# Kernel tuning notes

Hardware: AMD Instinct MI355X
Metric: run time of the kernel (lower is better)

## Reference

```python
import jax, jax.numpy as jnp
import numpy as np
from jax import lax

B, C, H, W = 32, 684, 16, 64
HID, A, CK, K = 256, 512, 512, 11


def setup_inputs() -> dict:
    key = jax.random.key(0)
    ks = jax.random.split(key, 12)
    s = 0.02
    return {
        "cnn_features": jax.random.normal(ks[0], (B, C, H, W), jnp.float32),
        "hidden": jax.random.normal(ks[1], (B, HID), jnp.float32),
        "alpha_sum": jax.random.uniform(ks[2], (B, 1, H, W), jnp.float32),
        "image_mask": jnp.ones((B, 1, H, W), jnp.float32),
        # hidden_weight: Linear(HID -> A)
        "Wh": jax.random.normal(ks[3], (A, HID), jnp.float32) * s,
        "bh": jnp.zeros((A,), jnp.float32),
        # encoder_feature_conv: Conv2d(C -> A, 1x1) == pointwise linear
        "Wec": jax.random.normal(ks[4], (A, C), jnp.float32) * s,
        "bec": jnp.zeros((A,), jnp.float32),
        # attention_conv: Conv2d(1 -> CK, 11x11, pad 5, no bias)
        "Wac": jax.random.normal(ks[5], (CK, 1, K, K), jnp.float32) * s,
        # attention_weight: Linear(CK -> A, no bias)
        "Waw": jax.random.normal(ks[6], (A, CK), jnp.float32) * s,
        # alpha_convert: Linear(A -> 1)
        "Wv": jax.random.normal(ks[7], (1, A), jnp.float32) * s,
        "bv": jnp.zeros((1,), jnp.float32),
    }


def reference(cnn_features, hidden, alpha_sum, image_mask,
              Wh, bh, Wec, bec, Wac, Waw, Wv, bv):
    # query = hidden_weight(hidden): [B, A]
    query = hidden @ Wh.T + bh
    # attention_conv(alpha_sum): [B, CK, H, W]
    ast = lax.conv_general_dilated(
        alpha_sum, Wac, window_strides=(1, 1),
        padding=[(K // 2, K // 2), (K // 2, K // 2)],
        dimension_numbers=("NCHW", "OIHW", "NCHW"))
    # attention_weight on permuted conv output: [B, H, W, A]
    coverage_alpha = jnp.einsum("bkhw,ak->bhwa", ast, Waw)
    # encoder_feature_conv (1x1 conv == pointwise linear): [B, H, W, A]
    cnn_trans = jnp.einsum("bchw,ac->bhwa", cnn_features, Wec) + bec
    # additive attention score
    alpha_score = jnp.tanh(query[:, None, None, :] + coverage_alpha + cnn_trans)
    # alpha_convert -> scalar energy per position: [B, H, W]
    energy = jnp.einsum("bhwa,a->bhw", alpha_score, Wv[0]) + bv[0]
    energy = energy - energy.max()  # global max-subtract as in original
    energy_exp = jnp.exp(energy) * image_mask[:, 0]
    denom = energy_exp.sum(axis=(-1, -2))[:, None, None] + 1e-10
    alpha = energy_exp / denom  # [B, H, W]
    alpha_sum_new = alpha[:, None, :, :] + alpha_sum  # [B, 1, H, W]
    # context: weighted spatial sum over features -> [B, C]
    context_vector = jnp.einsum("bhw,bchw->bc", alpha, cnn_features)
    return (context_vector, alpha, alpha_sum_new)
```

## Files before the change

### kernel.cpp

```cpp
#include <hip/hip_runtime.h>
#include <math.h>

#define Bn   32
#define Cn   684
#define Hn   16
#define Wn   64
#define HWn  1024
#define HIDn 256
#define An   512
#define KKn  121
#define CREAL 805
#define CPAD 832
#define NSTEP 26
#define NBLK 256

#define OUT_ALPHA 21888
#define OUT_ASUM  (21888 + 32768)

typedef short short8 __attribute__((ext_vector_type(8)));
typedef float floatx4 __attribute__((ext_vector_type(4)));

__device__ __forceinline__ unsigned short f2bf(float f) {
    union { float f; unsigned int i; } v; v.f = f;
    unsigned int i = v.i;
    return (unsigned short)((i + 0x7fffu + ((i >> 16) & 1u)) >> 16);
}
__device__ __forceinline__ unsigned int pack2bf(float v0, float v1) {
    unsigned int u0 = __float_as_uint(v0), u1 = __float_as_uint(v1);
    u0 = (u0 + 0x7fffu + ((u0 >> 16) & 1u)) >> 16;
    u1 = (u1 + 0x7fffu + ((u1 >> 16) & 1u)) & 0xffff0000u;
    return u0 | u1;
}
__device__ __forceinline__ void async_lds16(void* lds, const void* g) {
    __builtin_amdgcn_global_load_lds(
        (const __attribute__((address_space(1))) unsigned int*)g,
        (__attribute__((address_space(3))) unsigned int*)lds, 16, 0, 0);
}

__global__ __launch_bounds__(256) void k_prep(
    const float* __restrict__ hidden,
    const float* __restrict__ Wh,
    const float* __restrict__ bh,
    const float* __restrict__ bec,
    const float* __restrict__ Wec,
    const float* __restrict__ Wac,
    const float* __restrict__ Waw,
    float* __restrict__ query,
    unsigned short* __restrict__ VTbf)
{
    __shared__ float sbuf[512];
    const int blk = blockIdx.x, t = threadIdx.x;
    if (blk < 512) {
        const int a = blk;
        sbuf[t]       = Waw[(size_t)a * 512 + t];
        sbuf[t + 256] = Waw[(size_t)a * 512 + t + 256];
        __syncthreads();
        for (int cp = t; cp < Cn; cp += 256)
            VTbf[(size_t)a * CPAD + cp] = f2bf(Wec[(size_t)a * Cn + cp]);
        if (t < KKn) {
            float s = 0.f;
            #pragma unroll 8
            for (int k = 0; k < 512; ++k)
                s = fmaf(sbuf[k], Wac[k * KKn + t], s);
            VTbf[(size_t)a * CPAD + Cn + t] = f2bf(s);
        }
        for (int cp = CREAL + t; cp < CPAD; cp += 256)
            VTbf[(size_t)a * CPAD + cp] = 0;
    } else {
        const int b = blk - 512;
        sbuf[t] = (t < HIDn) ? hidden[b * HIDn + t] : 0.f;
        __syncthreads();
        for (int a = t; a < An; a += 256) {
            const float4* wp = (const float4*)(Wh + (size_t)a * HIDn);
            float s = bh[a] + bec[a];
            #pragma unroll 8
            for (int i = 0; i < HIDn / 4; ++i) {
                float4 w = wp[i];
                s = fmaf(sbuf[4 * i],     w.x, s);
                s = fmaf(sbuf[4 * i + 1], w.y, s);
                s = fmaf(sbuf[4 * i + 2], w.z, s);
                s = fmaf(sbuf[4 * i + 3], w.w, s);
            }
            query[b * An + a] = s;
        }
    }
}

__device__ __forceinline__ float fetchU(const float* __restrict__ X,
                                        const float* plane,
                                        int m, int row) {
    if (row < Cn)   return X[(size_t)row * HWn + m];
    if (row < CREAL) {
        int ij = row - Cn; int di = ij / 11, dj = ij - di * 11;
        return plane[di * 74 + m + dj];
    }
    return 0.f;
}

__global__ __launch_bounds__(256, 3) void k_energy(
    const float* __restrict__ X,
    const float* __restrict__ asum,
    const float* __restrict__ Wv,
    const float* __restrict__ query,
    const unsigned short* __restrict__ VTbf,
    float* __restrict__ energy)
{
    __shared__ __align__(16) unsigned short As[2 * 64 * 40];
    __shared__ __align__(16) unsigned short Bs[2 * 256 * 32];
    __shared__ float plane[11 * 74 + 2];
    __shared__ float qs[NBLK];
    __shared__ float wvs[NBLK];

    const int t = threadIdx.x;
    const int nh = blockIdx.x, hh = blockIdx.y, b = blockIdx.z;
    const int w = t >> 6, lane = t & 63;
    const int q = lane >> 4, r = lane & 15;
    const int nbase = nh * NBLK;
    const int mA = t & 63;
    const int koA = t >> 6;

    const float* Xb = X + (size_t)b * Cn * HWn + hh * Wn;

    const int gcw = (lane & 3) ^ ((lane >> 2) & 3) ^ ((lane >> 4) & 3);

    for (int i = t; i < 11 * 74; i += 256) {
        int di = i / 74, cc = i - di * 74;
        int h2 = hh + di - 5, w2 = cc - 5;
        float v = 0.f;
        if (h2 >= 0 && h2 < Hn && w2 >= 0 && w2 < Wn)
            v = asum[b * HWn + h2 * Wn + w2];
        plane[i] = v;
    }
    qs[t]  = query[b * An + nbase + t];
    wvs[t] = Wv[nbase + t];
    {
        const float* xp = Xb + (size_t)(koA * 8) * HWn + mA;
        unsigned int pk[4];
        #pragma unroll
        for (int jj = 0; jj < 4; ++jj)
            pk[jj] = pack2bf(xp[(size_t)(2 * jj) * HWn], xp[(size_t)(2 * jj + 1) * HWn]);
        *(uint4*)&As[mA * 40 + koA * 8] = make_uint4(pk[0], pk[1], pk[2], pk[3]);
    }
    #pragma unroll
    for (int ii = 0; ii < 4; ++ii) {
        int n0 = w * 64 + ii * 16;
        int row = nbase + n0 + (lane >> 2);
        async_lds16(&Bs[n0 * 32], VTbf + (size_t)row * CPAD + gcw * 8);
    }
    __syncthreads();

    floatx4 acc[4][4];
    #pragma unroll
    for (int mf = 0; mf < 4; ++mf)
        #pragma unroll
        for (int nf = 0; nf < 4; ++nf)
            acc[mf][nf] = (floatx4){0.f, 0.f, 0.f, 0.f};

    for (int ch = 0; ch < NSTEP; ++ch) {
        const int cur = ch & 1;
        const unsigned short* Ab = As + cur * (64 * 40);
        const unsigned short* Bb = Bs + cur * (256 * 32);

        short8 af[4], bfr[4];
        #pragma unroll
        for (int mf = 0; mf < 4; ++mf)
            af[mf] = *(const short8*)&Ab[(mf * 16 + r) * 40 + q * 8];
        #pragma unroll
        for (int nf = 0; nf < 4; ++nf)
            bfr[nf] = *(const short8*)&Bb[(w * 64 + nf * 16 + r) * 32 +
                                          ((q ^ (r & 3) ^ ((r >> 2) & 3)) * 8)];

        const bool stage = (ch < NSTEP - 1);
        float av[8];
        if (stage) {
            const int c1 = (ch + 1) * 32;
            if (c1 + 31 < Cn) {
                const float* xp = Xb + (size_t)(c1 + koA * 8) * HWn + mA;
                #pragma unroll
                for (int jj = 0; jj < 8; ++jj)
                    av[jj] = xp[(size_t)jj * HWn];
            } else {
                #pragma unroll
                for (int jj = 0; jj < 8; ++jj)
                    av[jj] = fetchU(Xb, plane, mA, c1 + koA * 8 + jj);
            }
            unsigned short* Bn_ = Bs + (cur ^ 1) * (256 * 32);
            #pragma unroll
            for (int ii = 0; ii < 4; ++ii) {
                int n0 = w * 64 + ii * 16;
                int row = nbase + n0 + (lane >> 2);
                async_lds16(&Bn_[n0 * 32], VTbf + (size_t)row * CPAD + c1 + gcw * 8);
            }
        }

        #pragma unroll
        for (int mf = 0; mf < 4; ++mf)
            #pragma unroll
            for (int nf = 0; nf < 4; ++nf)
                acc[mf][nf] = __builtin_amdgcn_mfma_f32_16x16x32_bf16(
                    af[mf], bfr[nf], acc[mf][nf], 0, 0, 0);

        if (stage) {
            unsigned int pk[4];
            #pragma unroll
            for (int jj = 0; jj < 4; ++jj)
                pk[jj] = pack2bf(av[2 * jj], av[2 * jj + 1]);
            *(uint4*)&As[(cur ^ 1) * (64 * 40) + mA * 40 + koA * 8] =
                make_uint4(pk[0], pk[1], pk[2], pk[3]);
        }

        __syncthreads();
    }

    float ep[16];
    #pragma unroll
    for (int i = 0; i < 16; ++i) ep[i] = 0.f;
    #pragma unroll
    for (int nf = 0; nf < 4; ++nf) {
        int nl = w * 64 + nf * 16 + r;
        float qv = qs[nl], wv = wvs[nl];
        #pragma unroll
        for (int mf = 0; mf < 4; ++mf)
            #pragma unroll
            for (int rg = 0; rg < 4; ++rg) {
                float x = acc[mf][nf][rg] + qv;
                float e2 = __expf(2.f * x);
                float th = 1.f - 2.f * __builtin_amdgcn_rcpf(e2 + 1.f);
                ep[mf * 4 + rg] += wv * th;
            }
    }
    float* red = (float*)Bs;
    #pragma unroll
    for (int mf = 0; mf < 4; ++mf)
        #pragma unroll
        for (int rg = 0; rg < 4; ++rg)
            red[(mf * 16 + q * 4 + rg) * 65 + w * 16 + r] = ep[mf * 4 + rg];
    __syncthreads();
    if (t < 64) {
        float s = 0.f;
        #pragma unroll 16
        for (int i = 0; i < 64; ++i) s += red[t * 65 + i];
        atomicAdd(&energy[b * HWn + hh * Wn + t], s);
    }
}

__global__ __launch_bounds__(256) void k_softmax(
    const float* __restrict__ mask,
    const float* __restrict__ asum,
    float* __restrict__ energy,
    float* __restrict__ out)
{
    __shared__ float rsm[8];
    const int b = blockIdx.x;
    const int t = threadIdx.x, lane = t & 63, wid = t >> 6;

    float e[4], ex[4];
    #pragma unroll
    for (int i = 0; i < 4; ++i) e[i] = energy[b * HWn + i * 256 + t];
    float m = fmaxf(fmaxf(e[0], e[1]), fmaxf(e[2], e[3]));
    for (int off = 32; off >= 1; off >>= 1) m = fmaxf(m, __shfl_down(m, off, 64));
    if (lane == 0) rsm[wid] = m;
    __syncthreads();
    if (t == 0)
        rsm[4] = fmaxf(fmaxf(rsm[0], rsm[1]), fmaxf(rsm[2], rsm[3]));
    __syncthreads();
    const float M = rsm[4];
    float s = 0.f;
    #pragma unroll
    for (int i = 0; i < 4; ++i) {
        ex[i] = expf(e[i] - M) * mask[b * HWn + i * 256 + t];
        s += ex[i];
    }
    for (int off = 32; off >= 1; off >>= 1) s += __shfl_down(s, off, 64);
    __syncthreads();
    if (lane == 0) rsm[wid] = s;
    __syncthreads();
    if (t == 0) rsm[5] = rsm[0] + rsm[1] + rsm[2] + rsm[3] + 1e-10f;
    __syncthreads();
    const float denom = rsm[5];
    #pragma unroll
    for (int i = 0; i < 4; ++i) {
        int p = i * 256 + t;
        float a = ex[i] / denom;
        energy[b * HWn + p] = a;
        out[OUT_ALPHA + b * HWn + p] = a;
        out[OUT_ASUM  + b * HWn + p] = a + asum[b * HWn + p];
    }
}

__global__ __launch_bounds__(256) void k_ctx(
    const float* __restrict__ X,
    const float* __restrict__ alpha,
    float* __restrict__ out)
{
    __shared__ float al[1024];
    const int bx = blockIdx.x, b = blockIdx.y;
    const int t = threadIdx.x, lane = t & 63, wid = t >> 6;

    #pragma unroll
    for (int i = 0; i < 4; ++i) al[i * 256 + t] = alpha[b * HWn + i * 256 + t];
    __syncthreads();

    const int c = bx * 4 + wid;
    const float* xp = X + ((size_t)(b * Cn + c)) * HWn;
    float s2 = 0.f;
    #pragma unroll
    for (int i = 0; i < 4; ++i) {
        int off = i * 256 + lane * 4;
        float4 x = *(const float4*)(xp + off);
        float4 a = *(const float4*)(al + off);
        s2 = fmaf(a.x, x.x, s2);
        s2 = fmaf(a.y, x.y, s2);
        s2 = fmaf(a.z, x.z, s2);
        s2 = fmaf(a.w, x.w, s2);
    }
    for (int off = 32; off >= 1; off >>= 1) s2 += __shfl_down(s2, off, 64);
    if (lane == 0) out[b * Cn + c] = s2;
}

extern "C" void kernel_launch(void* const* d_in, const int* in_sizes, int n_in,
                              void* d_out, int out_size, void* d_ws, size_t ws_size,
                              hipStream_t stream)
{
    const float* X      = (const float*)d_in[0];
    const float* hidden = (const float*)d_in[1];
    const float* asum   = (const float*)d_in[2];
    const float* mask   = (const float*)d_in[3];
    const float* Wh     = (const float*)d_in[4];
    const float* bh     = (const float*)d_in[5];
    const float* Wec    = (const float*)d_in[6];
    const float* bec    = (const float*)d_in[7];
    const float* Wac    = (const float*)d_in[8];
    const float* Waw    = (const float*)d_in[9];
    const float* Wv     = (const float*)d_in[10];
    (void)in_sizes; (void)n_in; (void)out_size; (void)ws_size;

    float* out = (float*)d_out;
    float* ws = (float*)d_ws;
    float* query  = ws;
    float* energy = ws + 16384;
    unsigned short* VTbf = (unsigned short*)(ws + 16384 + 32768);

    hipMemsetAsync(energy, 0, HWn * Bn * sizeof(float), stream);
    k_prep    <<<dim3(544),       dim3(256), 0, stream>>>(hidden, Wh, bh, bec,
                                                          Wec, Wac, Waw, query, VTbf);
    k_energy  <<<dim3(2, 16, 32), dim3(256), 0, stream>>>(X, asum, Wv, query, VTbf, energy);
    k_softmax <<<dim3(32),        dim3(256), 0, stream>>>(mask, asum, energy, out);
    k_ctx     <<<dim3(171, 32),   dim3(256), 0, stream>>>(X, energy, out);
}
```

Measured before the change: 272.6 us.

## Load B fragments directly from pre-swizzled global layout and remove block barriers

The prep kernel now writes the bf16 weight matrix in an MFMA fragment-ordered layout, so the energy kernel loads B fragments straight from global memory into registers instead of staging them through LDS. Each wave now stages its own copy of the A tile (all 64 positions by 32 channels) in a private LDS region, using float4 loads, which removes the per-step block-wide __syncthreads. The main loop is manually double-buffered in registers and LDS. The grid is flattened so the two N-halves of the same (b,h) tile run on adjacent blocks, sharing X reads through L2. The trade-off is four times the X loads and conversions per block, and more register pressure.

```diff
diff --git a/kernel.cpp b/kernel.cpp
--- a/kernel.cpp
+++ b/kernel.cpp
@@ -1,4 +1,5 @@
 #include <hip/hip_runtime.h>
+#include <hip/hip_bf16.h>
 #include <math.h>
 
 #define Bn   32
@@ -25,16 +26,15 @@
     unsigned int i = v.i;
     return (unsigned short)((i + 0x7fffu + ((i >> 16) & 1u)) >> 16);
 }
-__device__ __forceinline__ unsigned int pack2bf(float v0, float v1) {
-    unsigned int u0 = __float_as_uint(v0), u1 = __float_as_uint(v1);
-    u0 = (u0 + 0x7fffu + ((u0 >> 16) & 1u)) >> 16;
-    u1 = (u1 + 0x7fffu + ((u1 >> 16) & 1u)) & 0xffff0000u;
-    return u0 | u1;
-}
-__device__ __forceinline__ void async_lds16(void* lds, const void* g) {
-    __builtin_amdgcn_global_load_lds(
-        (const __attribute__((address_space(1))) unsigned int*)g,
-        (__attribute__((address_space(3))) unsigned int*)lds, 16, 0, 0);
+__device__ __forceinline__ unsigned int cvt2(float lo, float hi) {
+    __hip_bfloat162 h = __float22bfloat162_rn(float2{lo, hi});
+    union { __hip_bfloat162 h; unsigned int u; } cv; cv.h = h;
+    return cv.u;
+}
+
+__device__ __forceinline__ size_t bfr_idx(int n, int k) {
+    return ((((size_t)(n >> 4) * 26 + (k >> 5)) * 64
+             + ((k >> 3) & 3) * 16 + (n & 15)) * 8) + (k & 7);
 }
 
 __global__ __launch_bounds__(256) void k_prep(
@@ -46,7 +46,7 @@
     const float* __restrict__ Wac,
     const float* __restrict__ Waw,
     float* __restrict__ query,
-    unsigned short* __restrict__ VTbf)
+    unsigned short* __restrict__ Bfr)
 {
     __shared__ float sbuf[512];
     const int blk = blockIdx.x, t = threadIdx.x;
@@ -56,16 +56,16 @@
         sbuf[t + 256] = Waw[(size_t)a * 512 + t + 256];
         __syncthreads();
         for (int cp = t; cp < Cn; cp += 256)
-            VTbf[(size_t)a * CPAD + cp] = f2bf(Wec[(size_t)a * Cn + cp]);
+            Bfr[bfr_idx(a, cp)] = f2bf(Wec[(size_t)a * Cn + cp]);
         if (t < KKn) {
             float s = 0.f;
             #pragma unroll 8
             for (int k = 0; k < 512; ++k)
                 s = fmaf(sbuf[k], Wac[k * KKn + t], s);
-            VTbf[(size_t)a * CPAD + Cn + t] = f2bf(s);
+            Bfr[bfr_idx(a, Cn + t)] = f2bf(s);
         }
         for (int cp = CREAL + t; cp < CPAD; cp += 256)
-            VTbf[(size_t)a * CPAD + cp] = 0;
+            Bfr[bfr_idx(a, cp)] = 0;
     } else {
         const int b = blk - 512;
         sbuf[t] = (t < HIDn) ? hidden[b * HIDn + t] : 0.f;
@@ -86,42 +86,31 @@
     }
 }
 
-__device__ __forceinline__ float fetchU(const float* __restrict__ X,
-                                        const float* plane,
-                                        int m, int row) {
-    if (row < Cn)   return X[(size_t)row * HWn + m];
-    if (row < CREAL) {
-        int ij = row - Cn; int di = ij / 11, dj = ij - di * 11;
-        return plane[di * 74 + m + dj];
-    }
-    return 0.f;
-}
-
 __global__ __launch_bounds__(256, 3) void k_energy(
     const float* __restrict__ X,
     const float* __restrict__ asum,
     const float* __restrict__ Wv,
     const float* __restrict__ query,
-    const unsigned short* __restrict__ VTbf,
+    const unsigned short* __restrict__ Bfr,
     float* __restrict__ energy)
 {
-    __shared__ __align__(16) unsigned short As[2 * 64 * 40];
-    __shared__ __align__(16) unsigned short Bs[2 * 256 * 32];
+    __shared__ __align__(16) unsigned int As[4][2][64 * 20];
     __shared__ float plane[11 * 74 + 2];
     __shared__ float qs[NBLK];
     __shared__ float wvs[NBLK];
 
     const int t = threadIdx.x;
-    const int nh = blockIdx.x, hh = blockIdx.y, b = blockIdx.z;
+    const int d = blockIdx.x;
+    const int nh  = (d >> 3) & 1;
+    const int pid = (d >> 4) * 8 + (d & 7);
+    const int hh = pid & 15, b = pid >> 4;
     const int w = t >> 6, lane = t & 63;
     const int q = lane >> 4, r = lane & 15;
     const int nbase = nh * NBLK;
-    const int mA = t & 63;
-    const int koA = t >> 6;
+    const int mg = lane & 15, kg = lane >> 4;
 
     const float* Xb = X + (size_t)b * Cn * HWn + hh * Wn;
-
-    const int gcw = (lane & 3) ^ ((lane >> 2) & 3) ^ ((lane >> 4) & 3);
+    const unsigned short* Bp = Bfr + (size_t)(nh * 16 + w * 4) * 26 * 512;
 
     for (int i = t; i < 11 * 74; i += 256) {
         int di = i / 74, cc = i - di * 74;
@@ -133,21 +122,70 @@
     }
     qs[t]  = query[b * An + nbase + t];
     wvs[t] = Wv[nbase + t];
-    {
-        const float* xp = Xb + (size_t)(koA * 8) * HWn + mA;
-        unsigned int pk[4];
-        #pragma unroll
-        for (int jj = 0; jj < 4; ++jj)
-            pk[jj] = pack2bf(xp[(size_t)(2 * jj) * HWn], xp[(size_t)(2 * jj + 1) * HWn]);
-        *(uint4*)&As[mA * 40 + koA * 8] = make_uint4(pk[0], pk[1], pk[2], pk[3]);
-    }
-    #pragma unroll
-    for (int ii = 0; ii < 4; ++ii) {
-        int n0 = w * 64 + ii * 16;
-        int row = nbase + n0 + (lane >> 2);
-        async_lds16(&Bs[n0 * 32], VTbf + (size_t)row * CPAD + gcw * 8);
-    }
-    __syncthreads();
+    __syncthreads();
+
+    unsigned int* A0 = &As[w][0][0];
+    unsigned int* A1 = &As[w][1][0];
+
+    __align__(16) float va[32];
+    short8 b0[4], b1[4], af[4];
+
+#define LOADX(CH) {                                                           \
+    const int c0 = (CH) * 32 + kg * 8;                                        \
+    if (c0 + 7 < Cn) {                                                        \
+        const float* xp = Xb + (size_t)c0 * HWn + mg * 4;                     \
+        _Pragma("unroll")                                                     \
+        for (int j = 0; j < 8; ++j)                                           \
+            *(float4*)&va[j * 4] = *(const float4*)(xp + (size_t)j * HWn);    \
+    } else {                                                                  \
+        _Pragma("unroll")                                                     \
+        for (int j = 0; j < 8; ++j) {                                         \
+            const int row = c0 + j;                                           \
+            _Pragma("unroll")                                                 \
+            for (int mm = 0; mm < 4; ++mm) {                                  \
+                float vv = 0.f;                                               \
+                if (row < Cn) vv = Xb[(size_t)row * HWn + mg * 4 + mm];       \
+                else if (row < CREAL) {                                       \
+                    int ij = row - Cn; int di = ij / 11, dj = ij - di * 11;   \
+                    vv = plane[di * 74 + mg * 4 + mm + dj];                   \
+                }                                                             \
+                va[j * 4 + mm] = vv;                                          \
+            }                                                                 \
+        }                                                                     \
+    } }
+
+#define CVTWR(DST) {                                                          \
+    _Pragma("unroll")                                                         \
+    for (int mi = 0; mi < 4; ++mi) {                                          \
+        uint4 u;                                                              \
+        u.x = cvt2(va[0 * 4 + mi], va[1 * 4 + mi]);                           \
+        u.y = cvt2(va[2 * 4 + mi], va[3 * 4 + mi]);                           \
+        u.z = cvt2(va[4 * 4 + mi], va[5 * 4 + mi]);                           \
+        u.w = cvt2(va[6 * 4 + mi], va[7 * 4 + mi]);                           \
+        *(uint4*)&(DST)[(mg * 4 + mi) * 20 + kg * 4] = u;                     \
+    } }
+
+#define LOADB(DSTB, CH) {                                                     \
+    _Pragma("unroll")                                                         \
+    for (int nf = 0; nf < 4; ++nf)                                            \
+        DSTB[nf] = *(const short8*)(Bp + ((size_t)nf * 26 + (CH)) * 512       \
+                                       + lane * 8);                           \
+    }
+
+#define READA(SRC) {                                                          \
+    _Pragma("unroll")                                                         \
+    for (int mf = 0; mf < 4; ++mf)                                            \
+        af[mf] = *(const short8*)&(SRC)[(mf * 16 + r) * 20 + q * 4];          \
+    }
+
+#define MFMA16(BF) {                                                          \
+    _Pragma("unroll")                                                         \
+    for (int mf = 0; mf < 4; ++mf)                                            \
+        _Pragma("unroll")                                                     \
+        for (int nf = 0; nf < 4; ++nf)                                        \
+            acc[mf][nf] = __builtin_amdgcn_mfma_f32_16x16x32_bf16(            \
+                af[mf], BF[nf], acc[mf][nf], 0, 0, 0);                        \
+    }
 
     floatx4 acc[4][4];
     #pragma unroll
@@ -156,61 +194,26 @@
         for (int nf = 0; nf < 4; ++nf)
             acc[mf][nf] = (floatx4){0.f, 0.f, 0.f, 0.f};
 
-    for (int ch = 0; ch < NSTEP; ++ch) {
-        const int cur = ch & 1;
-        const unsigned short* Ab = As + cur * (64 * 40);
-        const unsigned short* Bb = Bs + cur * (256 * 32);
-
-        short8 af[4], bfr[4];
-        #pragma unroll
-        for (int mf = 0; mf < 4; ++mf)
-            af[mf] = *(const short8*)&Ab[(mf * 16 + r) * 40 + q * 8];
-        #pragma unroll
-        for (int nf = 0; nf < 4; ++nf)
-            bfr[nf] = *(const short8*)&Bb[(w * 64 + nf * 16 + r) * 32 +
-                                          ((q ^ (r & 3) ^ ((r >> 2) & 3)) * 8)];
-
-        const bool stage = (ch < NSTEP - 1);
-        float av[8];
-        if (stage) {
-            const int c1 = (ch + 1) * 32;
-            if (c1 + 31 < Cn) {
-                const float* xp = Xb + (size_t)(c1 + koA * 8) * HWn + mA;
-                #pragma unroll
-                for (int jj = 0; jj < 8; ++jj)
-                    av[jj] = xp[(size_t)jj * HWn];
-            } else {
-                #pragma unroll
-                for (int jj = 0; jj < 8; ++jj)
-                    av[jj] = fetchU(Xb, plane, mA, c1 + koA * 8 + jj);
-            }
-            unsigned short* Bn_ = Bs + (cur ^ 1) * (256 * 32);
-            #pragma unroll
-            for (int ii = 0; ii < 4; ++ii) {
-                int n0 = w * 64 + ii * 16;
-                int row = nbase + n0 + (lane >> 2);
-                async_lds16(&Bn_[n0 * 32], VTbf + (size_t)row * CPAD + c1 + gcw * 8);
-            }
-        }
-
-        #pragma unroll
-        for (int mf = 0; mf < 4; ++mf)
-            #pragma unroll
-            for (int nf = 0; nf < 4; ++nf)
-                acc[mf][nf] = __builtin_amdgcn_mfma_f32_16x16x32_bf16(
-                    af[mf], bfr[nf], acc[mf][nf], 0, 0, 0);
-
-        if (stage) {
-            unsigned int pk[4];
-            #pragma unroll
-            for (int jj = 0; jj < 4; ++jj)
-                pk[jj] = pack2bf(av[2 * jj], av[2 * jj + 1]);
-            *(uint4*)&As[(cur ^ 1) * (64 * 40) + mA * 40 + koA * 8] =
-                make_uint4(pk[0], pk[1], pk[2], pk[3]);
-        }
-
-        __syncthreads();
-    }
+    LOADX(0); CVTWR(A0);
+    LOADB(b0, 0);
+
+    for (int ch = 0; ch < NSTEP; ch += 2) {
+        LOADX(ch + 1);
+        LOADB(b1, ch + 1);
+        READA(A0);
+        MFMA16(b0);
+        CVTWR(A1);
+        if (ch + 2 < NSTEP) { LOADX(ch + 2); LOADB(b0, ch + 2); }
+        READA(A1);
+        MFMA16(b1);
+        if (ch + 2 < NSTEP) CVTWR(A0);
+    }
+
+#undef LOADX
+#undef CVTWR
+#undef LOADB
+#undef READA
+#undef MFMA16
 
     float ep[16];
     #pragma unroll
@@ -229,7 +232,8 @@
                 ep[mf * 4 + rg] += wv * th;
             }
     }
-    float* red = (float*)Bs;
+    __syncthreads();
+    float* red = (float*)As;
     #pragma unroll
     for (int mf = 0; mf < 4; ++mf)
         #pragma unroll
@@ -339,12 +343,12 @@
     float* ws = (float*)d_ws;
     float* query  = ws;
     float* energy = ws + 16384;
-    unsigned short* VTbf = (unsigned short*)(ws + 16384 + 32768);
+    unsigned short* Bfr = (unsigned short*)(ws + 16384 + 32768);
 
     hipMemsetAsync(energy, 0, HWn * Bn * sizeof(float), stream);
-    k_prep    <<<dim3(544),       dim3(256), 0, stream>>>(hidden, Wh, bh, bec,
-                                                          Wec, Wac, Waw, query, VTbf);
-    k_energy  <<<dim3(2, 16, 32), dim3(256), 0, stream>>>(X, asum, Wv, query, VTbf, energy);
-    k_softmax <<<dim3(32),        dim3(256), 0, stream>>>(mask, asum, energy, out);
-    k_ctx     <<<dim3(171, 32),   dim3(256), 0, stream>>>(X, energy, out);
-}
+    k_prep    <<<dim3(544),      dim3(256), 0, stream>>>(hidden, Wh, bh, bec,
+                                                         Wec, Wac, Waw, query, Bfr);
+    k_energy  <<<dim3(1024),     dim3(256), 0, stream>>>(X, asum, Wv, query, Bfr, energy);
+    k_softmax <<<dim3(32),       dim3(256), 0, stream>>>(mask, asum, energy, out);
+    k_ctx     <<<dim3(171, 32),  dim3(256), 0, stream>>>(X, energy, out);
+}
```

Result: slower. 284.8 us (+4.5%).

## Pre-swizzle B weights into MFMA fragment layout and load directly from global

Applied to the files above, without the earlier changes.

The prep kernel now writes the bf16 weight matrix in MFMA-fragment order, so each lane in the energy kernel can load its B operand straight from global memory with one 16-byte load. This drops the LDS staging buffer for B, which cuts LDS usage and lets occupancy rise to 4 blocks per CU. The grid is flattened to 1D and remapped so the two N-halves of the same (b, h) tile run in adjacent blocks for better L2 reuse of X. The final reduction uses wave shuffles instead of a padded LDS transpose. In exchange, B loads are no longer prefetched one step ahead, so their global latency may be exposed inside the loop.

```diff
diff --git a/kernel.cpp b/kernel.cpp
--- a/kernel.cpp
+++ b/kernel.cpp
@@ -1,4 +1,5 @@
 #include <hip/hip_runtime.h>
+#include <hip/hip_bf16.h>
 #include <math.h>
 
 #define Bn   32
@@ -25,16 +26,15 @@
     unsigned int i = v.i;
     return (unsigned short)((i + 0x7fffu + ((i >> 16) & 1u)) >> 16);
 }
-__device__ __forceinline__ unsigned int pack2bf(float v0, float v1) {
-    unsigned int u0 = __float_as_uint(v0), u1 = __float_as_uint(v1);
-    u0 = (u0 + 0x7fffu + ((u0 >> 16) & 1u)) >> 16;
-    u1 = (u1 + 0x7fffu + ((u1 >> 16) & 1u)) & 0xffff0000u;
-    return u0 | u1;
-}
-__device__ __forceinline__ void async_lds16(void* lds, const void* g) {
-    __builtin_amdgcn_global_load_lds(
-        (const __attribute__((address_space(1))) unsigned int*)g,
-        (__attribute__((address_space(3))) unsigned int*)lds, 16, 0, 0);
+__device__ __forceinline__ unsigned int cvt2(float lo, float hi) {
+    __hip_bfloat162 h = __float22bfloat162_rn(float2{lo, hi});
+    union { __hip_bfloat162 h; unsigned int u; } cv; cv.h = h;
+    return cv.u;
+}
+
+__device__ __forceinline__ size_t bfr_idx(int n, int k) {
+    return ((((size_t)(n >> 4) * 26 + (k >> 5)) * 64
+             + ((k >> 3) & 3) * 16 + (n & 15)) * 8) + (k & 7);
 }
 
 __global__ __launch_bounds__(256) void k_prep(
@@ -46,7 +46,7 @@
     const float* __restrict__ Wac,
     const float* __restrict__ Waw,
     float* __restrict__ query,
-    unsigned short* __restrict__ VTbf)
+    unsigned short* __restrict__ Bfr)
 {
     __shared__ float sbuf[512];
     const int blk = blockIdx.x, t = threadIdx.x;
@@ -56,16 +56,16 @@
         sbuf[t + 256] = Waw[(size_t)a * 512 + t + 256];
         __syncthreads();
         for (int cp = t; cp < Cn; cp += 256)
-            VTbf[(size_t)a * CPAD + cp] = f2bf(Wec[(size_t)a * Cn + cp]);
+            Bfr[bfr_idx(a, cp)] = f2bf(Wec[(size_t)a * Cn + cp]);
         if (t < KKn) {
             float s = 0.f;
             #pragma unroll 8
             for (int k = 0; k < 512; ++k)
                 s = fmaf(sbuf[k], Wac[k * KKn + t], s);
-            VTbf[(size_t)a * CPAD + Cn + t] = f2bf(s);
+            Bfr[bfr_idx(a, Cn + t)] = f2bf(s);
         }
         for (int cp = CREAL + t; cp < CPAD; cp += 256)
-            VTbf[(size_t)a * CPAD + cp] = 0;
+            Bfr[bfr_idx(a, cp)] = 0;
     } else {
         const int b = blk - 512;
         sbuf[t] = (t < HIDn) ? hidden[b * HIDn + t] : 0.f;
@@ -97,22 +97,25 @@
     return 0.f;
 }
 
-__global__ __launch_bounds__(256, 3) void k_energy(
+__global__ __launch_bounds__(256, 4) void k_energy(
     const float* __restrict__ X,
     const float* __restrict__ asum,
     const float* __restrict__ Wv,
     const float* __restrict__ query,
-    const unsigned short* __restrict__ VTbf,
+    const unsigned short* __restrict__ Bfr,
     float* __restrict__ energy)
 {
-    __shared__ __align__(16) unsigned short As[2 * 64 * 40];
-    __shared__ __align__(16) unsigned short Bs[2 * 256 * 32];
+    __shared__ __align__(16) unsigned short As[2][64 * 40];
     __shared__ float plane[11 * 74 + 2];
     __shared__ float qs[NBLK];
     __shared__ float wvs[NBLK];
+    __shared__ float red[4][64];
 
     const int t = threadIdx.x;
-    const int nh = blockIdx.x, hh = blockIdx.y, b = blockIdx.z;
+    const int d = blockIdx.x;
+    const int nh  = (d >> 3) & 1;
+    const int pid = (d >> 4) * 8 + (d & 7);
+    const int hh = pid & 15, b = pid >> 4;
     const int w = t >> 6, lane = t & 63;
     const int q = lane >> 4, r = lane & 15;
     const int nbase = nh * NBLK;
@@ -120,8 +123,7 @@
     const int koA = t >> 6;
 
     const float* Xb = X + (size_t)b * Cn * HWn + hh * Wn;
-
-    const int gcw = (lane & 3) ^ ((lane >> 2) & 3) ^ ((lane >> 4) & 3);
+    const unsigned short* Bp = Bfr + (size_t)(nh * 16 + w * 4) * 26 * 512;
 
     for (int i = t; i < 11 * 74; i += 256) {
         int di = i / 74, cc = i - di * 74;
@@ -135,17 +137,12 @@
     wvs[t] = Wv[nbase + t];
     {
         const float* xp = Xb + (size_t)(koA * 8) * HWn + mA;
-        unsigned int pk[4];
-        #pragma unroll
-        for (int jj = 0; jj < 4; ++jj)
-            pk[jj] = pack2bf(xp[(size_t)(2 * jj) * HWn], xp[(size_t)(2 * jj + 1) * HWn]);
-        *(uint4*)&As[mA * 40 + koA * 8] = make_uint4(pk[0], pk[1], pk[2], pk[3]);
-    }
-    #pragma unroll
-    for (int ii = 0; ii < 4; ++ii) {
-        int n0 = w * 64 + ii * 16;
-        int row = nbase + n0 + (lane >> 2);
-        async_lds16(&Bs[n0 * 32], VTbf + (size_t)row * CPAD + gcw * 8);
+        uint4 u;
+        u.x = cvt2(xp[0],              xp[(size_t)1 * HWn]);
+        u.y = cvt2(xp[(size_t)2 * HWn], xp[(size_t)3 * HWn]);
+        u.z = cvt2(xp[(size_t)4 * HWn], xp[(size_t)5 * HWn]);
+        u.w = cvt2(xp[(size_t)6 * HWn], xp[(size_t)7 * HWn]);
+        *(uint4*)&As[0][mA * 40 + koA * 8] = u;
     }
     __syncthreads();
 
@@ -158,39 +155,36 @@
 
     for (int ch = 0; ch < NSTEP; ++ch) {
         const int cur = ch & 1;
-        const unsigned short* Ab = As + cur * (64 * 40);
-        const unsigned short* Bb = Bs + cur * (256 * 32);
-
-        short8 af[4], bfr[4];
+
+        short8 bf[4];
+        #pragma unroll
+        for (int nf = 0; nf < 4; ++nf)
+            bf[nf] = *(const short8*)(Bp + ((size_t)(nf * 26 + ch)) * 512 + lane * 8);
+
+        short8 af[4];
         #pragma unroll
         for (int mf = 0; mf < 4; ++mf)
-            af[mf] = *(const short8*)&Ab[(mf * 16 + r) * 40 + q * 8];
-        #pragma unroll
-        for (int nf = 0; nf < 4; ++nf)
-            bfr[nf] = *(const short8*)&Bb[(w * 64 + nf * 16 + r) * 32 +
-                                          ((q ^ (r & 3) ^ ((r >> 2) & 3)) * 8)];
-
-        const bool stage = (ch < NSTEP - 1);
-        float av[8];
-        if (stage) {
-            const int c1 = (ch + 1) * 32;
-            if (c1 + 31 < Cn) {
-                const float* xp = Xb + (size_t)(c1 + koA * 8) * HWn + mA;
+            af[mf] = *(const short8*)&As[cur][(mf * 16 + r) * 40 + q * 8];
+
+        if (ch < NSTEP - 1) {
+            const int c0 = (ch + 1) * 32 + koA * 8;
+            float va[8];
+            if (c0 + 7 < Cn) {
+                const float* xp = Xb + (size_t)c0 * HWn + mA;
                 #pragma unroll
-                for (int jj = 0; jj < 8; ++jj)
-                    av[jj] = xp[(size_t)jj * HWn];
+                for (int j = 0; j < 8; ++j)
+                    va[j] = xp[(size_t)j * HWn];
             } else {
                 #pragma unroll
-                for (int jj = 0; jj < 8; ++jj)
-                    av[jj] = fetchU(Xb, plane, mA, c1 + koA * 8 + jj);
+                for (int j = 0; j < 8; ++j)
+                    va[j] = fetchU(Xb, plane, mA, c0 + j);
             }
-            unsigned short* Bn_ = Bs + (cur ^ 1) * (256 * 32);
-            #pragma unroll
-            for (int ii = 0; ii < 4; ++ii) {
-                int n0 = w * 64 + ii * 16;
-                int row = nbase + n0 + (lane >> 2);
-                async_lds16(&Bn_[n0 * 32], VTbf + (size_t)row * CPAD + c1 + gcw * 8);
-            }
+            uint4 u;
+            u.x = cvt2(va[0], va[1]);
+            u.y = cvt2(va[2], va[3]);
+            u.z = cvt2(va[4], va[5]);
+            u.w = cvt2(va[6], va[7]);
+            *(uint4*)&As[cur ^ 1][mA * 40 + koA * 8] = u;
         }
 
         #pragma unroll
@@ -198,16 +192,7 @@
             #pragma unroll
             for (int nf = 0; nf < 4; ++nf)
                 acc[mf][nf] = __builtin_amdgcn_mfma_f32_16x16x32_bf16(
-                    af[mf], bfr[nf], acc[mf][nf], 0, 0, 0);
-
-        if (stage) {
-            unsigned int pk[4];
-            #pragma unroll
-            for (int jj = 0; jj < 4; ++jj)
-                pk[jj] = pack2bf(av[2 * jj], av[2 * jj + 1]);
-            *(uint4*)&As[(cur ^ 1) * (64 * 40) + mA * 40 + koA * 8] =
-                make_uint4(pk[0], pk[1], pk[2], pk[3]);
-        }
+                    af[mf], bf[nf], acc[mf][nf], 0, 0, 0);
 
         __syncthreads();
     }
@@ -229,17 +214,22 @@
                 ep[mf * 4 + rg] += wv * th;
             }
     }
-    float* red = (float*)Bs;
-    #pragma unroll
-    for (int mf = 0; mf < 4; ++mf)
-        #pragma unroll
-        for (int rg = 0; rg < 4; ++rg)
-            red[(mf * 16 + q * 4 + rg) * 65 + w * 16 + r] = ep[mf * 4 + rg];
+    #pragma unroll
+    for (int i = 0; i < 16; ++i) {
+        #pragma unroll
+        for (int msk = 1; msk <= 8; msk <<= 1)
+            ep[i] += __shfl_xor(ep[i], msk, 64);
+    }
+    if (r == 0) {
+        #pragma unroll
+        for (int mf = 0; mf < 4; ++mf)
+            #pragma unroll
+            for (int rg = 0; rg < 4; ++rg)
+                red[w][mf * 16 + q * 4 + rg] = ep[mf * 4 + rg];
+    }
     __syncthreads();
     if (t < 64) {
-        float s = 0.f;
-        #pragma unroll 16
-        for (int i = 0; i < 64; ++i) s += red[t * 65 + i];
+        float s = red[0][t] + red[1][t] + red[2][t] + red[3][t];
         atomicAdd(&energy[b * HWn + hh * Wn + t], s);
     }
 }
@@ -339,12 +329,12 @@
     float* ws = (float*)d_ws;
     float* query  = ws;
     float* energy = ws + 16384;
-    unsigned short* VTbf = (unsigned short*)(ws + 16384 + 32768);
+    unsigned short* Bfr = (unsigned short*)(ws + 16384 + 32768);
 
     hipMemsetAsync(energy, 0, HWn * Bn * sizeof(float), stream);
-    k_prep    <<<dim3(544),       dim3(256), 0, stream>>>(hidden, Wh, bh, bec,
-                                                          Wec, Wac, Waw, query, VTbf);
-    k_energy  <<<dim3(2, 16, 32), dim3(256), 0, stream>>>(X, asum, Wv, query, VTbf, energy);
-    k_softmax <<<dim3(32),        dim3(256), 0, stream>>>(mask, asum, energy, out);
-    k_ctx     <<<dim3(171, 32),   dim3(256), 0, stream>>>(X, energy, out);
-}
+    k_prep    <<<dim3(544),      dim3(256), 0, stream>>>(hidden, Wh, bh, bec,
+                                                         Wec, Wac, Waw, query, Bfr);
+    k_energy  <<<dim3(1024),     dim3(256), 0, stream>>>(X, asum, Wv, query, Bfr, energy);
+    k_softmax <<<dim3(32),       dim3(256), 0, stream>>>(mask, asum, energy, out);
+    k_ctx     <<<dim3(171, 32),  dim3(256), 0, stream>>>(X, energy, out);
+}
```

Measured after the change: 262.2 us. -3.8%, faster.
